# Optimization experiments

Measured on AMD Instinct MI355X. Metric: run time of the kernel, lower is better.

The kernel has to match this reference:

```python
import jax, jax.numpy as jnp
import numpy as np

B, L, C, H, MAX_K, TAU = 64, 512, 256, 8, 512, 1.0
N = B * L
DH = C // H


def setup_inputs() -> dict:
    key = jax.random.key(0)
    ks = jax.random.split(key, 16)
    s = 0.02
    return {
        "x": jax.random.normal(ks[0], (N, C), jnp.float32),
        "edge_index": jax.random.randint(ks[1], (2, 200000), 0, N, jnp.int64),
        "batch": jnp.repeat(jnp.arange(B, dtype=jnp.int64), L),
        "token_ratio": jax.random.uniform(ks[2], (B,), jnp.float32, 0.05, 0.95),
        # gumbel = -log(Exp(1)) matches -empty.exponential_().log()
        "gumbel": -jnp.log(jax.random.exponential(ks[3], (B, L), jnp.float32)),
        # scorer: Linear(C,C) -> ReLU -> Linear(C,1)
        "Ws1": jax.random.normal(ks[4], (C, C), jnp.float32) * s,
        "bs1": jnp.zeros((C,), jnp.float32),
        "Ws2": jax.random.normal(ks[5], (1, C), jnp.float32) * s,
        "bs2": jnp.zeros((1,), jnp.float32),
        # MultiheadAttention packed in-proj [3C, C] and out-proj [C, C]
        "Win": jax.random.normal(ks[6], (3 * C, C), jnp.float32) * s,
        "b_in": jnp.zeros((3 * C,), jnp.float32),
        "Wout": jax.random.normal(ks[7], (C, C), jnp.float32) * s,
        "bout": jnp.zeros((C,), jnp.float32),
        # MLP: Linear(C, 2C) -> ReLU -> Linear(2C, C)
        "Wm1": jax.random.normal(ks[8], (2 * C, C), jnp.float32) * s,
        "bm1": jnp.zeros((2 * C,), jnp.float32),
        "Wm2": jax.random.normal(ks[9], (C, 2 * C), jnp.float32) * s,
        "bm2": jnp.zeros((C,), jnp.float32),
    }


def reference(x, edge_index, batch, token_ratio, gumbel,
              Ws1, bs1, Ws2, bs2, Win, b_in, Wout, bout, Wm1, bm1, Wm2, bm2):
    # conv=None, norm=None, eval mode (dropout = identity), equal-length graphs
    h_dense = x.reshape(B, L, C)                                  # to_dense_batch
    real_len = L                                                  # all graphs full
    k_per = jnp.clip(jnp.ceil(token_ratio * real_len).astype(jnp.int32),
                     1, min(MAX_K, L))                            # [B]
    k_max = int(np.max(np.asarray(k_per)))                        # concrete

    # scorer -> log-softmax scores (mask is all True, no -inf fill needed)
    s1 = jax.nn.relu(h_dense @ Ws1.T + bs1)
    scores = (s1 @ Ws2.T + bs2)[..., 0]                           # [B, L]
    log_scores = jax.nn.log_softmax(scores, axis=-1)

    # gumbel top-k with straight-through one-hot mask
    y_soft = jax.nn.softmax((log_scores + gumbel) / TAU, axis=-1)
    _, idx_g = jax.lax.top_k(y_soft, k_max)                       # [B, k_max]
    bidx = jnp.arange(B)[:, None]
    y_hard = jnp.zeros_like(y_soft).at[bidx, idx_g].set(1.0)
    token_mask = y_hard + y_soft - jax.lax.stop_gradient(y_soft)  # == y_hard numerically

    # sort descending, zero tokens beyond k_per[i], scatter back to node order
    sort_idx = jnp.argsort(-jax.lax.stop_gradient(token_mask), axis=-1, stable=True)
    sorted_mask = jnp.take_along_axis(token_mask, sort_idx, axis=1)
    keep = jnp.arange(L)[None, :] < k_per[:, None]
    sorted_mask = jnp.where(keep, sorted_mask, 0.0)
    refined = jnp.zeros_like(sorted_mask).at[bidx, sort_idx].set(sorted_mask)

    # compact gather + padded self-attention
    weighted = h_dense * refined[..., None]                       # [B, L, C]
    _, topk_idx = jax.lax.top_k(jax.lax.stop_gradient(refined), k_max)
    h_compact = jnp.take_along_axis(weighted, topk_idx[..., None], axis=1)  # [B,k,C]
    compact_mask = jnp.arange(k_max)[None, :] < k_per[:, None]    # [B, k]

    qkv = h_compact @ Win.T + b_in
    q, k, v = jnp.split(qkv, 3, axis=-1)
    hd = lambda t: t.reshape(B, k_max, H, DH)
    att = jnp.einsum('bqhd,bkhd->bhqk', hd(q), hd(k)) / np.sqrt(DH)
    att = jnp.where(compact_mask[:, None, None, :], att, -jnp.inf)
    att = jax.nn.softmax(att, axis=-1)
    h_attn = jnp.einsum('bhqk,bkhd->bqhd', att, hd(v)).reshape(B, k_max, C)
    h_attn = h_attn @ Wout.T + bout

    # scatter back to dense node positions
    h_full = jnp.zeros((B, L, C), x.dtype).at[bidx, topk_idx].set(h_attn)
    h = h_full.reshape(N, C) + x
    h = h * token_ratio[batch][:, None]

    out = h  # hs == [h] since conv is None
    out = out + (jax.nn.relu(out @ Wm1.T + bm1) @ Wm2.T + bm2)
    return out
```

## Files before the change

kernel.cpp:

```cpp
#include <hip/hip_runtime.h>
#include <hip/hip_bf16.h>
#include <math.h>

#define BB 64
#define LL 512
#define CC 256
#define HH 8
#define DHH 32
#define NN (BB * LL)

typedef __attribute__((ext_vector_type(8))) short bf16x8;
typedef __attribute__((ext_vector_type(4))) float f32x4;
typedef __attribute__((ext_vector_type(4))) unsigned short us4;

#define MFMA16(a, b, c) __builtin_amdgcn_mfma_f32_16x16x32_bf16(a, b, c, 0, 0, 0)

__device__ __forceinline__ unsigned short f2bf(float f) {
  unsigned u = __builtin_bit_cast(unsigned, f);
  u += 0x7fffu + ((u >> 16) & 1u);
  return (unsigned short)(u >> 16);
}
__device__ __forceinline__ float bf2f(unsigned short h) {
  unsigned u = ((unsigned)h) << 16;
  return __builtin_bit_cast(float, u);
}

__global__ __launch_bounds__(256) void k_cvt(
    const float* __restrict__ Ws1, unsigned short* __restrict__ W1h,
    unsigned short* __restrict__ W1l, const float* __restrict__ Win,
    unsigned short* __restrict__ Winh, const float* __restrict__ Wout,
    unsigned short* __restrict__ Wouth, const float* __restrict__ Wm1,
    unsigned short* __restrict__ Wm1h, const float* __restrict__ Wm2,
    unsigned short* __restrict__ Wm2h) {
  const int NW1 = CC * CC;
  const int NWIN = 3 * CC * CC;
  const int NWM = 2 * CC * CC;
  int i = blockIdx.x * 256 + threadIdx.x;
  if (i < NW1) {
    float v = Ws1[i];
    unsigned short hb = f2bf(v);
    W1h[i] = hb;
    W1l[i] = f2bf(v - bf2f(hb));
    return;
  }
  i -= NW1;
  if (i < NWIN) { Winh[i] = f2bf(Win[i]); return; }
  i -= NWIN;
  if (i < NW1) { Wouth[i] = f2bf(Wout[i]); return; }
  i -= NW1;
  if (i < NWM) { Wm1h[i] = f2bf(Wm1[i]); return; }
  i -= NWM;
  if (i < NWM) Wm2h[i] = f2bf(Wm2[i]);
}

__global__ __launch_bounds__(512, 4) void k_scorer(
    const float* __restrict__ x, unsigned short* __restrict__ xh,
    const unsigned short* __restrict__ W1h,
    const unsigned short* __restrict__ W1l, const float* __restrict__ bs1,
    const float* __restrict__ Ws2, const float* __restrict__ bs2,
    float* __restrict__ scores) {
  __shared__ unsigned short Ah[64][264];
  __shared__ unsigned short Al[64][264];
  __shared__ float red[8][64];
  int t = threadIdx.x;
  int tok0 = blockIdx.x * 64;
  int lane = t & 63, wid = t >> 6, quad = lane >> 4, l16 = lane & 15;
  bf16x8 bhc[2], blc[2];
#pragma unroll
  for (int nt = 0; nt < 2; ++nt) {
    int n = wid * 32 + nt * 16 + l16;
    bhc[nt] = *(const bf16x8*)&W1h[(size_t)n * CC + quad * 8];
    blc[nt] = *(const bf16x8*)&W1l[(size_t)n * CC + quad * 8];
  }
  for (int idx = t; idx < 64 * 64; idx += 512) {
    int r = idx >> 6, c4 = idx & 63;
    float4 v = *(const float4*)(x + (size_t)(tok0 + r) * CC + c4 * 4);
    float vv[4] = {v.x, v.y, v.z, v.w};
    unsigned short hb[4], lb[4];
#pragma unroll
    for (int j = 0; j < 4; ++j) {
      hb[j] = f2bf(vv[j]);
      lb[j] = f2bf(vv[j] - bf2f(hb[j]));
    }
    *(us4*)&Ah[r][c4 * 4] = *(us4*)hb;
    *(us4*)&Al[r][c4 * 4] = *(us4*)lb;
    ((us4*)(xh + (size_t)(tok0 + r) * CC))[c4] = *(us4*)hb;
  }
  __syncthreads();
  f32x4 acc[4][2] = {};
  for (int k0 = 0; k0 < CC; k0 += 32) {
    bf16x8 bhn[2], bln[2];
    bool more = (k0 + 32 < CC);
    if (more) {
#pragma unroll
      for (int nt = 0; nt < 2; ++nt) {
        int n = wid * 32 + nt * 16 + l16;
        bhn[nt] = *(const bf16x8*)&W1h[(size_t)n * CC + (k0 + 32) + quad * 8];
        bln[nt] = *(const bf16x8*)&W1l[(size_t)n * CC + (k0 + 32) + quad * 8];
      }
    }
    bf16x8 ah_[4], al_[4];
#pragma unroll
    for (int rt = 0; rt < 4; ++rt) {
      ah_[rt] = *(const bf16x8*)&Ah[rt * 16 + l16][k0 + quad * 8];
      al_[rt] = *(const bf16x8*)&Al[rt * 16 + l16][k0 + quad * 8];
    }
#pragma unroll
    for (int nt = 0; nt < 2; ++nt)
#pragma unroll
      for (int rt = 0; rt < 4; ++rt) {
        acc[rt][nt] = MFMA16(ah_[rt], bhc[nt], acc[rt][nt]);
        acc[rt][nt] = MFMA16(ah_[rt], blc[nt], acc[rt][nt]);
        acc[rt][nt] = MFMA16(al_[rt], bhc[nt], acc[rt][nt]);
      }
    if (more) {
#pragma unroll
      for (int nt = 0; nt < 2; ++nt) { bhc[nt] = bhn[nt]; blc[nt] = bln[nt]; }
    }
  }
  float rs[4][4] = {};
#pragma unroll
  for (int nt = 0; nt < 2; ++nt) {
    int n = wid * 32 + nt * 16 + l16;
    float b1 = bs1[n], w2 = Ws2[n];
#pragma unroll
    for (int rt = 0; rt < 4; ++rt)
#pragma unroll
      for (int r = 0; r < 4; ++r)
        rs[rt][r] += fmaxf(acc[rt][nt][r] + b1, 0.f) * w2;
  }
#pragma unroll
  for (int o = 1; o < 16; o <<= 1)
#pragma unroll
    for (int rt = 0; rt < 4; ++rt)
#pragma unroll
      for (int r = 0; r < 4; ++r) rs[rt][r] += __shfl_xor(rs[rt][r], o);
  if (l16 == 0) {
#pragma unroll
    for (int rt = 0; rt < 4; ++rt)
#pragma unroll
      for (int r = 0; r < 4; ++r)
        red[wid][rt * 16 + quad * 4 + r] = rs[rt][r];
  }
  __syncthreads();
  if (t < 64) {
    float s = bs2[0];
#pragma unroll
    for (int w = 0; w < 8; ++w) s += red[w][t];
    scores[tok0 + t] = s;
  }
}

__global__ __launch_bounds__(512) void k_presel(
    const float* __restrict__ scores, const float* __restrict__ gumbel,
    const float* __restrict__ ratio, int* __restrict__ k_per,
    int* __restrict__ codes, int* __restrict__ row2l,
    int* __restrict__ qkv_wl, int* __restrict__ qkv_cnt,
    int* __restrict__ atn_wl, int* __restrict__ atn_cnt) {
  __shared__ float zs[LL];
  __shared__ int sel[LL];
  __shared__ float red[8];
  __shared__ int kps[64];
  __shared__ int offq[65], offa[65];
  int b = blockIdx.x, l = threadIdx.x;
  int lane = l & 63, wid = l >> 6;
  if (l < 64) {
    int kp_ = (int)ceilf(ratio[l] * (float)LL);
    kp_ = min(max(kp_, 1), LL);
    kps[l] = kp_;
    if (l == b) k_per[b] = kp_;
  }
  __syncthreads();
  if (b == 0) {
    if (l == 0) {
      int oq = 0, oa = 0;
      for (int j = 0; j < 64; ++j) {
        int rj = (kps[j] < LL) ? kps[j] + 1 : LL;
        offq[j] = oq; offa[j] = oa;
        oq += (rj + 31) >> 5;
        oa += (rj + 127) >> 7;
      }
      offq[64] = oq; offa[64] = oa;
      qkv_cnt[0] = oq; atn_cnt[0] = oa;
    }
    __syncthreads();
    for (int j = 0; j < 64; ++j) {
      int nq = offq[j + 1] - offq[j];
      int na = offa[j + 1] - offa[j];
      if (l < nq) qkv_wl[offq[j] + l] = j * 16 + l;
      if (l < na) atn_wl[offa[j] + l] = j * 4 + l;
    }
  }
  int kp = kps[b];
  int km = 0;
#pragma unroll
  for (int j = 0; j < 64; ++j) km = max(km, kps[j]);
  float v = scores[b * LL + l];
  float m = v;
  for (int o = 32; o > 0; o >>= 1) m = fmaxf(m, __shfl_down(m, o));
  if (lane == 0) red[wid] = m;
  __syncthreads();
  m = red[0];
#pragma unroll
  for (int j = 1; j < 8; ++j) m = fmaxf(m, red[j]);
  __syncthreads();
  float e = expf(v - m);
  for (int o = 32; o > 0; o >>= 1) e += __shfl_down(e, o);
  if (lane == 0) red[wid] = e;
  __syncthreads();
  float tot = red[0];
#pragma unroll
  for (int j = 1; j < 8; ++j) tot += red[j];
  float lse = m + logf(tot);
  float zl = v - lse + gumbel[b * LL + l];
  zs[l] = zl;
  __syncthreads();
  int rank = 0;
  for (int j = 0; j < LL; ++j) {
    float zj = zs[j];
    rank += (zj > zl) || (zj == zl && j < l);
  }
  int s = (rank < km) ? 1 : 0;
  sel[l] = s;
  __syncthreads();
  int ps = 0;
  for (int j = 0; j < l; ++j) ps += sel[j];
  int kept = s && (ps < kp);
  int keptPrefix = min(ps, kp);
  int code;
  if (kept)
    code = ps;
  else if ((l - keptPrefix) < (km - kp))
    code = kp;
  else
    code = -1;
  codes[b * LL + l] = code;
  if (kept) row2l[b * LL + ps] = l;
}

__global__ __launch_bounds__(512, 2) void k_qkv(
    const unsigned short* __restrict__ xh, const int* __restrict__ row2l,
    const int* __restrict__ k_per, const unsigned short* __restrict__ Winh,
    const float* __restrict__ b_in, unsigned short* __restrict__ qh,
    unsigned short* __restrict__ kh, unsigned short* __restrict__ vh,
    const int* __restrict__ qkv_wl, const int* __restrict__ qkv_cnt) {
  int bid = blockIdx.x;
  if (bid >= qkv_cnt[0]) return;
  int wl = qkv_wl[bid];
  int b = wl >> 4, xchunk = wl & 15;
  int kp = k_per[b];
  int rows = (kp < LL) ? kp + 1 : LL;
  int r0 = xchunk * 32;
  __shared__ unsigned short A1[32][264];
  int t = threadIdx.x;
  int lane = t & 63, wid = t >> 6, quad = lane >> 4, row16 = lane & 15;

  bf16x8 bcur[6];
#pragma unroll
  for (int nt = 0; nt < 6; ++nt) {
    int n = wid * 96 + nt * 16 + row16;
    bcur[nt] = *(const bf16x8*)&Winh[(size_t)n * CC + quad * 8];
  }

  int c4 = t & 63, rr = t >> 6;
  int rl[4];
#pragma unroll
  for (int i = 0; i < 4; ++i) {
    int gr = r0 + rr + i * 8;
    rl[i] = (gr < kp) ? row2l[b * LL + gr] : -1;
  }
#pragma unroll
  for (int i = 0; i < 4; ++i) {
    us4 v = {0, 0, 0, 0};
    if (rl[i] >= 0)
      v = ((const us4*)(xh + ((size_t)b * LL + rl[i]) * CC))[c4];
    *(us4*)&A1[rr + i * 8][c4 * 4] = v;
  }
  __syncthreads();

  f32x4 acc[2][6] = {};
  for (int k0 = 0; k0 < CC; k0 += 32) {
    bf16x8 bnxt[6];
    bool more = (k0 + 32 < CC);
    if (more) {
#pragma unroll
      for (int nt = 0; nt < 6; ++nt) {
        int n = wid * 96 + nt * 16 + row16;
        bnxt[nt] = *(const bf16x8*)&Winh[(size_t)n * CC + (k0 + 32) + quad * 8];
      }
    }
    bf16x8 a0 = *(const bf16x8*)&A1[row16][k0 + quad * 8];
    bf16x8 a1 = *(const bf16x8*)&A1[16 + row16][k0 + quad * 8];
#pragma unroll
    for (int nt = 0; nt < 6; ++nt) {
      acc[0][nt] = MFMA16(a0, bcur[nt], acc[0][nt]);
      acc[1][nt] = MFMA16(a1, bcur[nt], acc[1][nt]);
    }
    if (more) {
#pragma unroll
      for (int nt = 0; nt < 6; ++nt) bcur[nt] = bnxt[nt];
    }
  }

#pragma unroll
  for (int p = 0; p < 3; ++p) {
    __syncthreads();
#pragma unroll
    for (int nt = 0; nt < 6; ++nt) {
      int n = wid * 96 + nt * 16 + row16;
      if ((n >> 8) == p) {
        int nc = n & 255;
        float bias = b_in[n];
#pragma unroll
        for (int rt = 0; rt < 2; ++rt)
#pragma unroll
          for (int r = 0; r < 4; ++r)
            A1[rt * 16 + quad * 4 + r][nc] = f2bf(acc[rt][nt][r] + bias);
      }
    }
    __syncthreads();
    unsigned short* dst = (p == 0) ? qh : (p == 1) ? kh : vh;
#pragma unroll
    for (int i = 0; i < 2; ++i) {
      int flat = i * 512 + t;
      int row = flat >> 5, c16 = flat & 31;
      int grow = r0 + row;
      if (grow < rows)
        *(bf16x8*)(dst + ((size_t)b * LL + grow) * CC + c16 * 8) =
            *(const bf16x8*)&A1[row][c16 * 8];
    }
  }
}

__global__ __launch_bounds__(256, 4) void k_attn(
    const unsigned short* __restrict__ qh, const unsigned short* __restrict__ kh,
    const unsigned short* __restrict__ vh, const int* __restrict__ k_per,
    unsigned short* __restrict__ ah,
    const int* __restrict__ atn_wl, const int* __restrict__ atn_cnt) {
  int bid = blockIdx.x;
  if (bid >= atn_cnt[0]) return;
  int wl = atn_wl[bid];
  int b = wl >> 2, qi = wl & 3;
  int h = blockIdx.y;
  int kp = k_per[b];
  int rows = (kp < LL) ? kp + 1 : LL;
  int q0 = qi * 128;
  int t = threadIdx.x;
  int lane = t & 63, wid = t >> 6, quad = lane >> 4, l16 = lane & 15;

  __shared__ unsigned short Kc[128 * 40];
  __shared__ unsigned short Vt[32 * 132];
  __shared__ unsigned short Pb[4][16 * 132];

  size_t base = ((size_t)b * LL) * CC + (size_t)h * DHH;

  bf16x8 aQ[2] = {};
  f32x4 o0[2] = {}, o1[2] = {}, o2[2] = {};
#pragma unroll
  for (int g = 0; g < 2; ++g) {
    int myq = q0 + wid * 32 + g * 16 + l16;
    if (myq < rows)
      aQ[g] = *(const bf16x8*)(qh + base + (size_t)myq * CC + quad * 8);
  }
  bf16x8 vone;
#pragma unroll
  for (int j = 0; j < 8; ++j) vone[j] = (short)0x3F80;

  const float scale = 0.17677669529663687f;
  int nch = (kp + 127) >> 7;
  unsigned short* Pw = Pb[wid];

  int kK0 = t >> 2;
  int kc8 = (t & 3) * 8;
  int vd0 = (t & 7) * 4;
  int vk0 = (t >> 3) * 4;

  bf16x8 Kreg[2];
  us4 Vreg[4];
  auto LOADC = [&](int cc) {
    int kb = cc << 7;
#pragma unroll
    for (int i = 0; i < 2; ++i) {
      int gk = kb + kK0 + i * 64;
      bf16x8 z = {};
      if (gk < kp) z = *(const bf16x8*)(kh + base + (size_t)gk * CC + kc8);
      Kreg[i] = z;
    }
#pragma unroll
    for (int i = 0; i < 4; ++i) {
      int gk = kb + vk0 + i;
      us4 z4 = {0, 0, 0, 0};
      if (gk < kp) z4 = *(const us4*)(vh + base + (size_t)gk * CC + vd0);
      Vreg[i] = z4;
    }
  };

  LOADC(0);
  for (int c = 0; c < nch; ++c) {
    int kbase = c << 7;
    __syncthreads();
    *(bf16x8*)&Kc[kK0 * 40 + kc8] = Kreg[0];
    *(bf16x8*)&Kc[(kK0 + 64) * 40 + kc8] = Kreg[1];
#pragma unroll
    for (int j = 0; j < 4; ++j) {
      us4 w = {Vreg[0][j], Vreg[1][j], Vreg[2][j], Vreg[3][j]};
      *(us4*)&Vt[(vd0 + j) * 132 + vk0] = w;
    }
    __syncthreads();
    if (c + 1 < nch) LOADC(c + 1);
#pragma unroll
    for (int g = 0; g < 2; ++g) {
      f32x4 s[8];
      __builtin_amdgcn_s_setprio(1);
#pragma unroll
      for (int tt = 0; tt < 8; ++tt) {
        f32x4 z4 = {};
        bf16x8 bK = *(const bf16x8*)&Kc[(tt * 16 + l16) * 40 + quad * 8];
        s[tt] = MFMA16(aQ[g], bK, z4);
      }
      __builtin_amdgcn_s_setprio(0);
#pragma unroll
      for (int tt = 0; tt < 8; ++tt) {
        float sb = (kbase + tt * 16 + l16 < kp) ? 0.f : -1e30f;
#pragma unroll
        for (int r = 0; r < 4; ++r) s[tt][r] = __expf(fmaf(s[tt][r], scale, sb));
      }
#pragma unroll
      for (int tt = 0; tt < 8; ++tt)
#pragma unroll
        for (int r = 0; r < 4; ++r)
          Pw[(quad * 4 + r) * 132 + tt * 16 + l16] = f2bf(s[tt][r]);
      __builtin_amdgcn_s_setprio(1);
#pragma unroll
      for (int gg = 0; gg < 4; ++gg) {
        if (kbase + gg * 32 < kp) {
          bf16x8 aP = *(const bf16x8*)&Pw[l16 * 132 + gg * 32 + quad * 8];
          int koff = gg * 32 + quad * 8;
          struct U8 { us4 a, bq; };
          U8 u0, u1;
          u0.a = *(const us4*)&Vt[l16 * 132 + koff];
          u0.bq = *(const us4*)&Vt[l16 * 132 + koff + 4];
          u1.a = *(const us4*)&Vt[(16 + l16) * 132 + koff];
          u1.bq = *(const us4*)&Vt[(16 + l16) * 132 + koff + 4];
          o0[g] = MFMA16(aP, __builtin_bit_cast(bf16x8, u0), o0[g]);
          o1[g] = MFMA16(aP, __builtin_bit_cast(bf16x8, u1), o1[g]);
          o2[g] = MFMA16(aP, vone, o2[g]);
        }
      }
      __builtin_amdgcn_s_setprio(0);
    }
  }

  unsigned short (*Ob)[40] = (unsigned short(*)[40]) & Pb[0][0];
  __syncthreads();
#pragma unroll
  for (int g = 0; g < 2; ++g)
#pragma unroll
    for (int r = 0; r < 4; ++r) {
      int ql = wid * 32 + g * 16 + quad * 4 + r;
      float invl = 1.f / o2[g][r];
      Ob[ql][l16] = f2bf(o0[g][r] * invl);
      Ob[ql][16 + l16] = f2bf(o1[g][r] * invl);
    }
  __syncthreads();
#pragma unroll
  for (int i = 0; i < 2; ++i) {
    int flat = i * 256 + t;
    int ql = flat >> 2, c = flat & 3;
    int q = q0 + ql;
    if (q < rows)
      *(bf16x8*)(ah + base + (size_t)q * CC + c * 8) =
          *(const bf16x8*)&Ob[ql][c * 8];
  }
}

__global__ __launch_bounds__(512, 4) void k_opmlp(
    const unsigned short* __restrict__ ah, const int* __restrict__ codes,
    const unsigned short* __restrict__ Wouth, const float* __restrict__ bout,
    const unsigned short* __restrict__ xh, const float* __restrict__ ratio,
    const unsigned short* __restrict__ Wm1h, const float* __restrict__ bm1,
    const unsigned short* __restrict__ Wm2h, const float* __restrict__ bm2,
    float* __restrict__ out) {
  int b = blockIdx.y;
  int l0 = blockIdx.x * 64;
  int t = threadIdx.x;
  __shared__ unsigned short A1[64][264];
  __shared__ unsigned short Hs[64][264];
  __shared__ int cd[64];
  if (t < 64) cd[t] = codes[b * LL + l0 + t];
  __syncthreads();
  for (int idx = t; idx < 64 * 64; idx += 512) {
    int r = idx >> 6, c4 = idx & 63;
    int c = cd[r];
    us4 v = {0, 0, 0, 0};
    if (c >= 0) v = ((const us4*)(ah + ((size_t)b * LL + c) * CC))[c4];
    *(us4*)&A1[r][c4 * 4] = v;
  }
  int lane = t & 63, wid = t >> 6, quad = lane >> 4, l16 = lane & 15;
  bf16x8 bcur[2];
#pragma unroll
  for (int nt = 0; nt < 2; ++nt)
    bcur[nt] =
        *(const bf16x8*)&Wouth[(size_t)(wid * 32 + nt * 16 + l16) * CC + quad * 8];
  unsigned short xv[4][2][4];
#pragma unroll
  for (int rt = 0; rt < 4; ++rt)
#pragma unroll
    for (int nt = 0; nt < 2; ++nt) {
      int n = wid * 32 + nt * 16 + l16;
#pragma unroll
      for (int r = 0; r < 4; ++r)
        xv[rt][nt][r] =
            xh[((size_t)b * LL + l0 + rt * 16 + quad * 4 + r) * CC + n];
    }
  __syncthreads();

  f32x4 acc[4][2] = {};
  for (int k0 = 0; k0 < CC; k0 += 32) {
    bf16x8 bnxt[2];
    bool more = (k0 + 32 < CC);
    if (more) {
#pragma unroll
      for (int nt = 0; nt < 2; ++nt)
        bnxt[nt] = *(const bf16x8*)&Wouth[(size_t)(wid * 32 + nt * 16 + l16) * CC +
                                          (k0 + 32) + quad * 8];
    }
    bf16x8 a_[4];
#pragma unroll
    for (int rt = 0; rt < 4; ++rt)
      a_[rt] = *(const bf16x8*)&A1[rt * 16 + l16][k0 + quad * 8];
#pragma unroll
    for (int nt = 0; nt < 2; ++nt)
#pragma unroll
      for (int rt = 0; rt < 4; ++rt)
        acc[rt][nt] = MFMA16(a_[rt], bcur[nt], acc[rt][nt]);
    if (more) { bcur[0] = bnxt[0]; bcur[1] = bnxt[1]; }
  }
  float rt_ratio = ratio[b];
  f32x4 acc2[4][2];
#pragma unroll
  for (int rt = 0; rt < 4; ++rt)
#pragma unroll
    for (int nt = 0; nt < 2; ++nt) {
      int n = wid * 32 + nt * 16 + l16;
      float bias = bout[n];
#pragma unroll
      for (int r = 0; r < 4; ++r) {
        int rl = rt * 16 + quad * 4 + r;
        int c = cd[rl];
        float y = (c >= 0) ? (acc[rt][nt][r] + bias) : 0.f;
        acc2[rt][nt][r] = (y + bf2f(xv[rt][nt][r])) * rt_ratio;
      }
    }
  __syncthreads();
#pragma unroll
  for (int rt = 0; rt < 4; ++rt)
#pragma unroll
    for (int nt = 0; nt < 2; ++nt) {
      int n = wid * 32 + nt * 16 + l16;
#pragma unroll
      for (int r = 0; r < 4; ++r)
        A1[rt * 16 + quad * 4 + r][n] = f2bf(acc2[rt][nt][r]);
    }
  __syncthreads();

#pragma unroll
  for (int half = 0; half < 2; ++half) {
    f32x4 acc1[4][2] = {};
    bf16x8 c1[2];
#pragma unroll
    for (int nt = 0; nt < 2; ++nt)
      c1[nt] = *(const bf16x8*)&Wm1h[(size_t)(half * 256 + wid * 32 + nt * 16 +
                                              l16) * CC + quad * 8];
    for (int k0 = 0; k0 < CC; k0 += 32) {
      bf16x8 n1[2];
      bool more = (k0 + 32 < CC);
      if (more) {
#pragma unroll
        for (int nt = 0; nt < 2; ++nt)
          n1[nt] = *(const bf16x8*)&Wm1h[(size_t)(half * 256 + wid * 32 +
                                                  nt * 16 + l16) * CC +
                                         (k0 + 32) + quad * 8];
      }
      bf16x8 a_[4];
#pragma unroll
      for (int rt = 0; rt < 4; ++rt)
        a_[rt] = *(const bf16x8*)&A1[rt * 16 + l16][k0 + quad * 8];
#pragma unroll
      for (int nt = 0; nt < 2; ++nt)
#pragma unroll
        for (int rt = 0; rt < 4; ++rt)
          acc1[rt][nt] = MFMA16(a_[rt], c1[nt], acc1[rt][nt]);
      if (more) { c1[0] = n1[0]; c1[1] = n1[1]; }
    }
    if (half == 1) __syncthreads();
#pragma unroll
    for (int rt = 0; rt < 4; ++rt)
#pragma unroll
      for (int nt = 0; nt < 2; ++nt) {
        int hc = wid * 32 + nt * 16 + l16;
        float bias = bm1[half * 256 + hc];
#pragma unroll
        for (int r = 0; r < 4; ++r) {
          float v = fmaxf(acc1[rt][nt][r] + bias, 0.f);
          Hs[rt * 16 + quad * 4 + r][hc] = f2bf(v);
        }
      }
    bf16x8 c2[2];
#pragma unroll
    for (int nt = 0; nt < 2; ++nt)
      c2[nt] = *(const bf16x8*)&Wm2h[(size_t)(wid * 32 + nt * 16 + l16) *
                                         (2 * CC) + half * 256 + quad * 8];
    __syncthreads();
    for (int k0 = 0; k0 < CC; k0 += 32) {
      bf16x8 n2[2];
      bool more = (k0 + 32 < CC);
      if (more) {
#pragma unroll
        for (int nt = 0; nt < 2; ++nt)
          n2[nt] = *(const bf16x8*)&Wm2h[(size_t)(wid * 32 + nt * 16 + l16) *
                                             (2 * CC) + half * 256 + (k0 + 32) +
                                         quad * 8];
      }
      bf16x8 h_[4];
#pragma unroll
      for (int rt = 0; rt < 4; ++rt)
        h_[rt] = *(const bf16x8*)&Hs[rt * 16 + l16][k0 + quad * 8];
#pragma unroll
      for (int nt = 0; nt < 2; ++nt)
#pragma unroll
        for (int rt = 0; rt < 4; ++rt)
          acc2[rt][nt] = MFMA16(h_[rt], c2[nt], acc2[rt][nt]);
      if (more) { c2[0] = n2[0]; c2[1] = n2[1]; }
    }
  }
#pragma unroll
  for (int rt = 0; rt < 4; ++rt)
#pragma unroll
    for (int nt = 0; nt < 2; ++nt) {
      int n = wid * 32 + nt * 16 + l16;
      float bias = bm2[n];
#pragma unroll
      for (int r = 0; r < 4; ++r) {
        int rl = rt * 16 + quad * 4 + r;
        size_t o = ((size_t)b * LL + l0 + rl) * CC + n;
        out[o] = acc2[rt][nt][r] + bias;
      }
    }
}

extern "C" void kernel_launch(void* const* d_in, const int* in_sizes, int n_in,
                              void* d_out, int out_size, void* d_ws,
                              size_t ws_size, hipStream_t stream) {
  (void)in_sizes; (void)n_in; (void)out_size; (void)ws_size;
  const float* x     = (const float*)d_in[0];
  const float* ratio = (const float*)d_in[3];
  const float* gum   = (const float*)d_in[4];
  const float* Ws1   = (const float*)d_in[5];
  const float* bs1   = (const float*)d_in[6];
  const float* Ws2   = (const float*)d_in[7];
  const float* bs2   = (const float*)d_in[8];
  const float* Win   = (const float*)d_in[9];
  const float* b_in  = (const float*)d_in[10];
  const float* Wout  = (const float*)d_in[11];
  const float* bout  = (const float*)d_in[12];
  const float* Wm1   = (const float*)d_in[13];
  const float* bm1   = (const float*)d_in[14];
  const float* Wm2   = (const float*)d_in[15];
  const float* bm2   = (const float*)d_in[16];
  float* out = (float*)d_out;

  const size_t NXC = (size_t)NN * CC;
  float* z    = (float*)d_ws;
  int* k_per  = (int*)(z + NN);
  int* codes  = k_per + 128;
  int* row2l  = codes + NN;
  unsigned short* xh    = (unsigned short*)(row2l + NN);
  unsigned short* qh    = xh + NXC;
  unsigned short* kh    = qh + NXC;
  unsigned short* vh    = kh + NXC;
  unsigned short* ahb   = vh + NXC;
  unsigned short* Winh  = ahb + NXC;
  unsigned short* Wouth = Winh + 3 * CC * CC;
  unsigned short* Wm1h  = Wouth + CC * CC;
  unsigned short* Wm2h  = Wm1h + 2 * CC * CC;
  unsigned short* W1h   = Wm2h + 2 * CC * CC;
  unsigned short* W1l   = W1h + CC * CC;
  int* qkv_wl  = (int*)(W1l + CC * CC);
  int* qkv_cnt = qkv_wl + 1024;
  int* atn_wl  = qkv_cnt + 1;
  int* atn_cnt = atn_wl + 256;

  const int cvt_total = 9 * CC * CC;
  k_cvt<<<(cvt_total + 255) / 256, 256, 0, stream>>>(
      Ws1, W1h, W1l, Win, Winh, Wout, Wouth, Wm1, Wm1h, Wm2, Wm2h);

  k_scorer<<<NN / 64, 512, 0, stream>>>(x, xh, W1h, W1l, bs1, Ws2, bs2, z);
  k_presel<<<BB, 512, 0, stream>>>(z, gum, ratio, k_per, codes, row2l,
                                   qkv_wl, qkv_cnt, atn_wl, atn_cnt);
  k_qkv<<<1024, 512, 0, stream>>>(xh, row2l, k_per, Winh, b_in, qh, kh, vh,
                                  qkv_wl, qkv_cnt);
  k_attn<<<dim3(256, HH), 256, 0, stream>>>(qh, kh, vh, k_per, ahb,
                                            atn_wl, atn_cnt);
  k_opmlp<<<dim3(8, BB), 512, 0, stream>>>(ahb, codes, Wouth, bout, xh, ratio,
                                           Wm1h, bm1, Wm2h, bm2, out);
}
```

Baseline: 305.5 us.

## Fuse weight conversion and preselection into scorer kernel via last-block atomic

Removes the separate weight-conversion kernel and the preselection kernel. Each scorer block now converts a slice of the attention and MLP weights to bf16, splits Ws1 into hi/lo bf16 on the fly from fp32, and the last of the eight blocks per graph (found with an atomic counter) runs the softmax, Gumbel ranking and worklist build. This saves two launches at the cost of a memset, redundant Ws1 conversion in every block, and a serialized tail in the last block of each graph.

```diff
diff --git a/kernel.cpp b/kernel.cpp
--- a/kernel.cpp
+++ b/kernel.cpp
@@ -25,53 +25,58 @@
   return __builtin_bit_cast(float, u);
 }
 
-__global__ __launch_bounds__(256) void k_cvt(
-    const float* __restrict__ Ws1, unsigned short* __restrict__ W1h,
-    unsigned short* __restrict__ W1l, const float* __restrict__ Win,
-    unsigned short* __restrict__ Winh, const float* __restrict__ Wout,
-    unsigned short* __restrict__ Wouth, const float* __restrict__ Wm1,
-    unsigned short* __restrict__ Wm1h, const float* __restrict__ Wm2,
-    unsigned short* __restrict__ Wm2h) {
-  const int NW1 = CC * CC;
-  const int NWIN = 3 * CC * CC;
-  const int NWM = 2 * CC * CC;
-  int i = blockIdx.x * 256 + threadIdx.x;
-  if (i < NW1) {
-    float v = Ws1[i];
-    unsigned short hb = f2bf(v);
-    W1h[i] = hb;
-    W1l[i] = f2bf(v - bf2f(hb));
-    return;
-  }
-  i -= NW1;
-  if (i < NWIN) { Winh[i] = f2bf(Win[i]); return; }
-  i -= NWIN;
-  if (i < NW1) { Wouth[i] = f2bf(Wout[i]); return; }
-  i -= NW1;
-  if (i < NWM) { Wm1h[i] = f2bf(Wm1[i]); return; }
-  i -= NWM;
-  if (i < NWM) Wm2h[i] = f2bf(Wm2[i]);
-}
-
 __global__ __launch_bounds__(512, 4) void k_scorer(
     const float* __restrict__ x, unsigned short* __restrict__ xh,
-    const unsigned short* __restrict__ W1h,
-    const unsigned short* __restrict__ W1l, const float* __restrict__ bs1,
+    const float* __restrict__ Ws1, const float* __restrict__ bs1,
     const float* __restrict__ Ws2, const float* __restrict__ bs2,
-    float* __restrict__ scores) {
+    float* __restrict__ z, const float* __restrict__ gumbel,
+    const float* __restrict__ ratio, int* __restrict__ k_per,
+    int* __restrict__ codes, int* __restrict__ row2l,
+    int* __restrict__ qkv_wl, int* __restrict__ qkv_cnt,
+    int* __restrict__ atn_wl, int* __restrict__ atn_cnt,
+    int* __restrict__ cnt,
+    const float* __restrict__ Win, unsigned short* __restrict__ Winh,
+    const float* __restrict__ Wout, unsigned short* __restrict__ Wouth,
+    const float* __restrict__ Wm1, unsigned short* __restrict__ Wm1h,
+    const float* __restrict__ Wm2, unsigned short* __restrict__ Wm2h) {
   __shared__ unsigned short Ah[64][264];
   __shared__ unsigned short Al[64][264];
   __shared__ float red[8][64];
+  __shared__ int lastFlag;
   int t = threadIdx.x;
   int tok0 = blockIdx.x * 64;
+  int b = blockIdx.x >> 3;
   int lane = t & 63, wid = t >> 6, quad = lane >> 4, l16 = lane & 15;
+
+  {
+    int i0 = blockIdx.x * 1024 + t;
+#pragma unroll
+    for (int j = 0; j < 2; ++j) {
+      int i = i0 + j * 512;
+      if (i < 196608) Winh[i] = f2bf(Win[i]);
+      else if (i < 262144) Wouth[i - 196608] = f2bf(Wout[i - 196608]);
+      else if (i < 393216) Wm1h[i - 262144] = f2bf(Wm1[i - 262144]);
+      else Wm2h[i - 393216] = f2bf(Wm2[i - 393216]);
+    }
+  }
+
+  auto ldw1 = [&](int n, int k, bf16x8& hi, bf16x8& lo) {
+    const float* p = Ws1 + (size_t)n * CC + k;
+    float4 a = *(const float4*)p, c = *(const float4*)(p + 4);
+    float vv[8] = {a.x, a.y, a.z, a.w, c.x, c.y, c.z, c.w};
+#pragma unroll
+    for (int j = 0; j < 8; ++j) {
+      unsigned short h = f2bf(vv[j]);
+      hi[j] = (short)h;
+      lo[j] = (short)f2bf(vv[j] - bf2f(h));
+    }
+  };
+
   bf16x8 bhc[2], blc[2];
 #pragma unroll
-  for (int nt = 0; nt < 2; ++nt) {
-    int n = wid * 32 + nt * 16 + l16;
-    bhc[nt] = *(const bf16x8*)&W1h[(size_t)n * CC + quad * 8];
-    blc[nt] = *(const bf16x8*)&W1l[(size_t)n * CC + quad * 8];
-  }
+  for (int nt = 0; nt < 2; ++nt)
+    ldw1(wid * 32 + nt * 16 + l16, 0, bhc[nt], blc[nt]);
+
   for (int idx = t; idx < 64 * 64; idx += 512) {
     int r = idx >> 6, c4 = idx & 63;
     float4 v = *(const float4*)(x + (size_t)(tok0 + r) * CC + c4 * 4);
@@ -93,11 +98,8 @@
     bool more = (k0 + 32 < CC);
     if (more) {
 #pragma unroll
-      for (int nt = 0; nt < 2; ++nt) {
-        int n = wid * 32 + nt * 16 + l16;
-        bhn[nt] = *(const bf16x8*)&W1h[(size_t)n * CC + (k0 + 32) + quad * 8];
-        bln[nt] = *(const bf16x8*)&W1l[(size_t)n * CC + (k0 + 32) + quad * 8];
-      }
+      for (int nt = 0; nt < 2; ++nt)
+        ldw1(wid * 32 + nt * 16 + l16, k0 + 32, bhn[nt], bln[nt]);
     }
     bf16x8 ah_[4], al_[4];
 #pragma unroll
@@ -147,27 +149,27 @@
     float s = bs2[0];
 #pragma unroll
     for (int w = 0; w < 8; ++w) s += red[w][t];
-    scores[tok0 + t] = s;
-  }
-}
-
-__global__ __launch_bounds__(512) void k_presel(
-    const float* __restrict__ scores, const float* __restrict__ gumbel,
-    const float* __restrict__ ratio, int* __restrict__ k_per,
-    int* __restrict__ codes, int* __restrict__ row2l,
-    int* __restrict__ qkv_wl, int* __restrict__ qkv_cnt,
-    int* __restrict__ atn_wl, int* __restrict__ atn_cnt) {
-  __shared__ float zs[LL];
-  __shared__ int sel[LL];
-  __shared__ float red[8];
-  __shared__ int kps[64];
-  __shared__ int offq[65], offa[65];
-  int b = blockIdx.x, l = threadIdx.x;
-  int lane = l & 63, wid = l >> 6;
+    z[tok0 + t] = s;
+  }
+
+  __threadfence();
+  __syncthreads();
+  if (t == 0) lastFlag = (atomicAdd(&cnt[b], 1) == 7);
+  __syncthreads();
+  if (!lastFlag) return;
+  __threadfence();
+
+  float* zs  = (float*)&Ah[0][0];
+  int*   sel = (int*)&Ah[16][0];
+  int*   kpsS = (int*)&Al[0][0];
+  float* red8 = (float*)&Al[2][0];
+  int*   offq = (int*)&Al[4][0];
+  int*   offa = (int*)&Al[8][0];
+  int l = t;
   if (l < 64) {
     int kp_ = (int)ceilf(ratio[l] * (float)LL);
     kp_ = min(max(kp_, 1), LL);
-    kps[l] = kp_;
+    kpsS[l] = kp_;
     if (l == b) k_per[b] = kp_;
   }
   __syncthreads();
@@ -175,7 +177,7 @@
     if (l == 0) {
       int oq = 0, oa = 0;
       for (int j = 0; j < 64; ++j) {
-        int rj = (kps[j] < LL) ? kps[j] + 1 : LL;
+        int rj = (kpsS[j] < LL) ? kpsS[j] + 1 : LL;
         offq[j] = oq; offa[j] = oa;
         oq += (rj + 31) >> 5;
         oa += (rj + 127) >> 7;
@@ -191,26 +193,26 @@
       if (l < na) atn_wl[offa[j] + l] = j * 4 + l;
     }
   }
-  int kp = kps[b];
+  int kp = kpsS[b];
   int km = 0;
 #pragma unroll
-  for (int j = 0; j < 64; ++j) km = max(km, kps[j]);
-  float v = scores[b * LL + l];
+  for (int j = 0; j < 64; ++j) km = max(km, kpsS[j]);
+  float v = z[b * LL + l];
   float m = v;
   for (int o = 32; o > 0; o >>= 1) m = fmaxf(m, __shfl_down(m, o));
-  if (lane == 0) red[wid] = m;
-  __syncthreads();
-  m = red[0];
-#pragma unroll
-  for (int j = 1; j < 8; ++j) m = fmaxf(m, red[j]);
+  if ((l & 63) == 0) red8[l >> 6] = m;
+  __syncthreads();
+  m = red8[0];
+#pragma unroll
+  for (int j = 1; j < 8; ++j) m = fmaxf(m, red8[j]);
   __syncthreads();
   float e = expf(v - m);
   for (int o = 32; o > 0; o >>= 1) e += __shfl_down(e, o);
-  if (lane == 0) red[wid] = e;
-  __syncthreads();
-  float tot = red[0];
-#pragma unroll
-  for (int j = 1; j < 8; ++j) tot += red[j];
+  if ((l & 63) == 0) red8[l >> 6] = e;
+  __syncthreads();
+  float tot = red8[0];
+#pragma unroll
+  for (int j = 1; j < 8; ++j) tot += red8[j];
   float lse = m + logf(tot);
   float zl = v - lse + gumbel[b * LL + l];
   zs[l] = zl;
@@ -382,9 +384,9 @@
 #pragma unroll
     for (int i = 0; i < 2; ++i) {
       int gk = kb + kK0 + i * 64;
-      bf16x8 z = {};
-      if (gk < kp) z = *(const bf16x8*)(kh + base + (size_t)gk * CC + kc8);
-      Kreg[i] = z;
+      bf16x8 zz = {};
+      if (gk < kp) zz = *(const bf16x8*)(kh + base + (size_t)gk * CC + kc8);
+      Kreg[i] = zz;
     }
 #pragma unroll
     for (int i = 0; i < 4; ++i) {
@@ -690,14 +692,14 @@
   int* qkv_cnt = qkv_wl + 1024;
   int* atn_wl  = qkv_cnt + 1;
   int* atn_cnt = atn_wl + 256;
-
-  const int cvt_total = 9 * CC * CC;
-  k_cvt<<<(cvt_total + 255) / 256, 256, 0, stream>>>(
-      Ws1, W1h, W1l, Win, Winh, Wout, Wouth, Wm1, Wm1h, Wm2, Wm2h);
-
-  k_scorer<<<NN / 64, 512, 0, stream>>>(x, xh, W1h, W1l, bs1, Ws2, bs2, z);
-  k_presel<<<BB, 512, 0, stream>>>(z, gum, ratio, k_per, codes, row2l,
-                                   qkv_wl, qkv_cnt, atn_wl, atn_cnt);
+  int* cnt     = atn_cnt + 1;
+
+  hipMemsetAsync(cnt, 0, 64 * sizeof(int), stream);
+
+  k_scorer<<<NN / 64, 512, 0, stream>>>(
+      x, xh, Ws1, bs1, Ws2, bs2, z, gum, ratio, k_per, codes, row2l,
+      qkv_wl, qkv_cnt, atn_wl, atn_cnt, cnt,
+      Win, Winh, Wout, Wouth, Wm1, Wm1h, Wm2, Wm2h);
   k_qkv<<<1024, 512, 0, stream>>>(xh, row2l, k_per, Winh, b_in, qh, kh, vh,
                                   qkv_wl, qkv_cnt);
   k_attn<<<dim3(256, HH), 256, 0, stream>>>(qh, kh, vh, k_per, ahb,
```

New measurement: 376.2 us. +23.1%, slower.
